# Optimization experiments

Measured on AMD Instinct MI355X. Metric: run time of the kernel, lower is better.

The kernel has to match this reference:

```python
import jax, jax.numpy as jnp
import numpy as np

DIM = 4096          # power of two -> no padding branch
LAYERS = 12         # log2(DIM)
BATCH = 8192


def setup_inputs() -> dict:
    key = jax.random.key(0)
    kx, ka = jax.random.split(key)
    x = jax.random.normal(kx, (BATCH, DIM), dtype=jnp.float32)
    # original init: uniform(-0.05, 0.05) per layer of DIM//2 angles
    angles = jax.random.uniform(ka, (LAYERS, DIM // 2), dtype=jnp.float32,
                                minval=-0.05, maxval=0.05)
    return {"x": x, "angles": angles}


def reference(x, angles):
    """Butterfly O(d log d) rotation. x:(B,d), angles:(L, d//2).

    Layer l pairs elements (j, j+stride), stride=2**l. The torch code's
    angle index for pair offset i in block starting at `start` is
    start//2 + i, which equals reshaping theta to (num_blocks, stride).
    """
    B, d = x.shape
    out = x
    for l in range(LAYERS):
        stride = 1 << l
        nb = d // (2 * stride)              # blocks per layer
        theta = angles[l].reshape(nb, stride)
        c = jnp.cos(theta)                  # (nb, stride)
        s = jnp.sin(theta)
        o = out.reshape(B, nb, 2, stride)
        xl = o[:, :, 0, :]                  # (B, nb, stride)
        xr = o[:, :, 1, :]
        new_l = c * xl + s * xr
        new_r = -s * xl + c * xr
        out = jnp.stack([new_l, new_r], axis=2).reshape(B, d)
    return out
```

## Files before the change

### kernel.cpp

```cpp
#include <hip/hip_runtime.h>
#include <hip/hip_fp16.h>


#define DIM    4096
#define LAYERS 12
#define BATCH  8192
#define NANG   2048
#define BLOCK  512

typedef unsigned int u32;
typedef float v2f __attribute__((ext_vector_type(2)));

#define BAR() do {                                             \
    asm volatile("s_waitcnt lgkmcnt(0)" ::: "memory");         \
    __builtin_amdgcn_sched_barrier(0);                         \
    __builtin_amdgcn_s_barrier();                              \
} while (0)

__device__ __forceinline__ int swzQ(int Q) {
    return Q ^ ((Q >> 3) & 7) ^ ((Q >> 6) & 7);
}
__device__ __forceinline__ int uslot(int e) {
    return 2 * swzQ(e >> 1) + (e & 1);
}
__device__ __forceinline__ constexpr int inner_idx(int m, int jj) {
    return ((m >> (jj + 1)) << jj) + (m & ((1 << jj) - 1));
}

__device__ __forceinline__ void rot2(v2f& xl, v2f& xr, float c, float s) {
    v2f nl = c * xl + s * xr;
    v2f nr = c * xr - s * xl;
    xl = nl; xr = nr;
}

__global__ void __launch_bounds__(256) cs_kernel(const float* __restrict__ angles,
                                                 u32* __restrict__ TH, int n) {
    int i = blockIdx.x * blockDim.x + threadIdx.x;
    if (i >= n) return;
    float a = angles[i];
    float c = cosf(a), s = sinf(a);
    int l = i >> 11, aa = i & 2047;
    int region, jj, t, ii;
    if (l < 3)      { region = 0; jj = l;     t = aa >> 2;  ii = aa & 3; }
    else if (l < 6) { region = 1; jj = l - 3; int B = aa >> 5, r = aa & 31;
                      ii = r >> 3; t = 8 * B + (r & 7); }
    else if (l < 9) { region = 2; jj = l - 6; int S = aa >> 8, r = aa & 255;
                      ii = r >> 6; t = 64 * S + (r & 63); }
    else            { region = 3; jj = l - 9; ii = aa >> 9; t = aa & 511; }
    int a_idx = jj * 4 + ii;
    int flat = ((region * 3 + (a_idx >> 2)) * 512 + t) * 4 + (a_idx & 3);
    u32 lo = (u32)__half_as_ushort(__float2half(1.0f - c));
    u32 hi = (u32)__half_as_ushort(__float2half(s));
    TH[flat] = lo | (hi << 16);
}

#define UNPACK_ANGLES(U0, U1, U2, ca, sa) do {                             \
    const u32 _u[12] = {U0.x, U0.y, U0.z, U0.w, U1.x, U1.y, U1.z, U1.w,    \
                        U2.x, U2.y, U2.z, U2.w};                           \
    _Pragma("unroll")                                                      \
    for (int a = 0; a < 12; ++a) {                                         \
        __half2 h2 = *reinterpret_cast<const __half2*>(&_u[a]);            \
        float2 f = __half22float2(h2);                                     \
        ca[a] = 1.0f - f.x;                                                \
        sa[a] = f.y;                                                       \
    }                                                                      \
} while (0)

#define PHASE_ROTS(ca, sa, w)                                              \
    _Pragma("unroll")                                                      \
    for (int jj = 0; jj < 3; ++jj) {                                       \
        const int st = 1 << jj;                                            \
        _Pragma("unroll")                                                  \
        for (int m = 0; m < 8; ++m) {                                      \
            if (!(m & st)) {                                               \
                const int a = jj * 4 + inner_idx(m, jj);                   \
                rot2(w[m], w[m + st], ca[a], sa[a]);                       \
            }                                                              \
        }                                                                  \
    }

__global__ void __launch_bounds__(BLOCK, 6)
butterfly_kernel(const float* __restrict__ x, const uint4* __restrict__ TH4,
                 float* __restrict__ out) {
    __shared__ v2f buf[DIM];
    const int t = threadIdx.x;
    const long row0 = (long)blockIdx.x * 2;

    v2f w[8];
    float ca[12], sa[12];

    {
        uint4 A0 = TH4[0 * 512 + t], A1 = TH4[1 * 512 + t], A2 = TH4[2 * 512 + t];
        const float* p0 = x + row0 * DIM + 8 * t;
        const float* p1 = p0 + DIM;
        float4 a = *(const float4*)(p0),     b = *(const float4*)(p0 + 4);
        float4 c = *(const float4*)(p1),     d = *(const float4*)(p1 + 4);
        uint4 B0 = TH4[3 * 512 + t], B1 = TH4[4 * 512 + t], B2 = TH4[5 * 512 + t];

        w[0] = v2f{a.x, c.x}; w[1] = v2f{a.y, c.y};
        w[2] = v2f{a.z, c.z}; w[3] = v2f{a.w, c.w};
        w[4] = v2f{b.x, d.x}; w[5] = v2f{b.y, d.y};
        w[6] = v2f{b.z, d.z}; w[7] = v2f{b.w, d.w};
        UNPACK_ANGLES(A0, A1, A2, ca, sa);
        PHASE_ROTS(ca, sa, w)
        #pragma unroll
        for (int q = 0; q < 4; ++q) {
            *(float4*)(&buf[2 * swzQ(4 * t + q)]) =
                make_float4(w[2*q].x, w[2*q].y, w[2*q+1].x, w[2*q+1].y);
        }
        BAR();

        uint4 C0 = TH4[6 * 512 + t], C1 = TH4[7 * 512 + t], C2 = TH4[8 * 512 + t];
        {
            const int eb = 64 * (t >> 3) + (t & 7);
            int ps[8];
            #pragma unroll
            for (int m = 0; m < 8; ++m) {
                ps[m] = uslot(eb + 8 * m);
                w[m] = buf[ps[m]];
            }
            UNPACK_ANGLES(B0, B1, B2, ca, sa);
            PHASE_ROTS(ca, sa, w)
            #pragma unroll
            for (int m = 0; m < 8; ++m) buf[ps[m]] = w[m];
        }
        BAR();

        uint4 D0 = TH4[9 * 512 + t], D1 = TH4[10 * 512 + t], D2 = TH4[11 * 512 + t];
        {
            const int eb = 512 * (t >> 6) + (t & 63);
            int ps[8];
            #pragma unroll
            for (int m = 0; m < 8; ++m) {
                ps[m] = uslot(eb + 64 * m);
                w[m] = buf[ps[m]];
            }
            UNPACK_ANGLES(C0, C1, C2, ca, sa);
            PHASE_ROTS(ca, sa, w)
            #pragma unroll
            for (int m = 0; m < 8; ++m) buf[ps[m]] = w[m];
        }
        BAR();

        {
            #pragma unroll
            for (int m = 0; m < 8; ++m) w[m] = buf[uslot(t + 512 * m)];
            UNPACK_ANGLES(D0, D1, D2, ca, sa);
            PHASE_ROTS(ca, sa, w)
            float* o0 = out + row0 * DIM + t;
            float* o1 = o0 + DIM;
            #pragma unroll
            for (int m = 0; m < 8; ++m) {
                o0[m << 9] = w[m].x;
                o1[m << 9] = w[m].y;
            }
        }
    }
}

extern "C" void kernel_launch(void* const* d_in, const int* in_sizes, int n_in,
                              void* d_out, int out_size, void* d_ws, size_t ws_size,
                              hipStream_t stream) {
    (void)in_sizes; (void)n_in; (void)out_size; (void)ws_size;
    const float* x      = (const float*)d_in[0];
    const float* angles = (const float*)d_in[1];
    float* out = (float*)d_out;

    const int n = LAYERS * NANG;
    cs_kernel<<<(n + 255) / 256, 256, 0, stream>>>(angles, (u32*)d_ws, n);
    butterfly_kernel<<<BATCH / 2, BLOCK, 0, stream>>>(x, (const uint4*)d_ws, out);
}
```

Baseline: 53.15 us.

## Use 16 elements per thread with 256-thread blocks and three LDS phases

Each thread now holds 16 two-row elements instead of 8, so each register phase covers four butterfly layers instead of three. The kernel needs three phases and two barriers instead of four phases and three, which cuts LDS round trips. Blocks shrink to 256 threads, and the angle table is re-laid out into 8 uint4 groups per phase. The rotation now uses the packed 1-cos value directly rather than rebuilding cos. More registers per thread lower the occupancy target from 6 to 4 blocks.

```diff
diff --git a/kernel.cpp b/kernel.cpp
--- a/kernel.cpp
+++ b/kernel.cpp
@@ -6,7 +6,7 @@
 #define LAYERS 12
 #define BATCH  8192
 #define NANG   2048
-#define BLOCK  512
+#define BLOCK  256
 
 typedef unsigned int u32;
 typedef float v2f __attribute__((ext_vector_type(2)));
@@ -27,9 +27,11 @@
     return ((m >> (jj + 1)) << jj) + (m & ((1 << jj) - 1));
 }
 
-__device__ __forceinline__ void rot2(v2f& xl, v2f& xr, float c, float s) {
-    v2f nl = c * xl + s * xr;
-    v2f nr = c * xr - s * xl;
+__device__ __forceinline__ void rot2d(v2f& xl, v2f& xr, float d, float s) {
+    v2f cl = xl - d * xl;
+    v2f cr = xr - d * xr;
+    v2f nl = cl + s * xr;
+    v2f nr = cr - s * xl;
     xl = nl; xr = nr;
 }
 
@@ -41,119 +43,107 @@
     float c = cosf(a), s = sinf(a);
     int l = i >> 11, aa = i & 2047;
     int region, jj, t, ii;
-    if (l < 3)      { region = 0; jj = l;     t = aa >> 2;  ii = aa & 3; }
-    else if (l < 6) { region = 1; jj = l - 3; int B = aa >> 5, r = aa & 31;
-                      ii = r >> 3; t = 8 * B + (r & 7); }
-    else if (l < 9) { region = 2; jj = l - 6; int S = aa >> 8, r = aa & 255;
-                      ii = r >> 6; t = 64 * S + (r & 63); }
-    else            { region = 3; jj = l - 9; ii = aa >> 9; t = aa & 511; }
-    int a_idx = jj * 4 + ii;
-    int flat = ((region * 3 + (a_idx >> 2)) * 512 + t) * 4 + (a_idx & 3);
+    if (l < 4)      { region = 0; jj = l;     t = aa >> 3; ii = aa & 7; }
+    else if (l < 8) { region = 1; jj = l - 4; int hi = aa >> 7, r = aa & 127;
+                      ii = r >> 4; t = hi + 16 * (r & 15); }
+    else            { region = 2; jj = l - 8; ii = aa >> 8; t = aa & 255; }
+    int group = region * 8 + jj * 2 + (ii >> 2);
+    int flat = (group * 256 + t) * 4 + (ii & 3);
     u32 lo = (u32)__half_as_ushort(__float2half(1.0f - c));
     u32 hi = (u32)__half_as_ushort(__float2half(s));
     TH[flat] = lo | (hi << 16);
 }
 
-#define UNPACK_ANGLES(U0, U1, U2, ca, sa) do {                             \
-    const u32 _u[12] = {U0.x, U0.y, U0.z, U0.w, U1.x, U1.y, U1.z, U1.w,    \
-                        U2.x, U2.y, U2.z, U2.w};                           \
+#define UNPACK8(Ua, Ub, dd, ss) do {                                       \
+    const u32 _u[8] = {Ua.x, Ua.y, Ua.z, Ua.w, Ub.x, Ub.y, Ub.z, Ub.w};    \
     _Pragma("unroll")                                                      \
-    for (int a = 0; a < 12; ++a) {                                         \
+    for (int a = 0; a < 8; ++a) {                                          \
         __half2 h2 = *reinterpret_cast<const __half2*>(&_u[a]);            \
         float2 f = __half22float2(h2);                                     \
-        ca[a] = 1.0f - f.x;                                                \
-        sa[a] = f.y;                                                       \
+        dd[a] = f.x; ss[a] = f.y;                                          \
     }                                                                      \
 } while (0)
 
-#define PHASE_ROTS(ca, sa, w)                                              \
+#define PHASE_ROTS(U, w)                                                   \
     _Pragma("unroll")                                                      \
-    for (int jj = 0; jj < 3; ++jj) {                                       \
+    for (int jj = 0; jj < 4; ++jj) {                                       \
+        float dd[8], ss[8];                                                \
+        UNPACK8(U[2*jj], U[2*jj+1], dd, ss);                               \
         const int st = 1 << jj;                                            \
         _Pragma("unroll")                                                  \
-        for (int m = 0; m < 8; ++m) {                                      \
+        for (int m = 0; m < 16; ++m) {                                     \
             if (!(m & st)) {                                               \
-                const int a = jj * 4 + inner_idx(m, jj);                   \
-                rot2(w[m], w[m + st], ca[a], sa[a]);                       \
+                rot2d(w[m], w[m + st], dd[inner_idx(m, jj)],               \
+                      ss[inner_idx(m, jj)]);                               \
             }                                                              \
         }                                                                  \
     }
 
-__global__ void __launch_bounds__(BLOCK, 6)
+__global__ void __launch_bounds__(BLOCK, 4)
 butterfly_kernel(const float* __restrict__ x, const uint4* __restrict__ TH4,
                  float* __restrict__ out) {
     __shared__ v2f buf[DIM];
     const int t = threadIdx.x;
     const long row0 = (long)blockIdx.x * 2;
 
-    v2f w[8];
-    float ca[12], sa[12];
+    v2f w[16];
+    uint4 U[8];
 
     {
-        uint4 A0 = TH4[0 * 512 + t], A1 = TH4[1 * 512 + t], A2 = TH4[2 * 512 + t];
-        const float* p0 = x + row0 * DIM + 8 * t;
+        const float* p0 = x + row0 * DIM + 16 * t;
         const float* p1 = p0 + DIM;
-        float4 a = *(const float4*)(p0),     b = *(const float4*)(p0 + 4);
-        float4 c = *(const float4*)(p1),     d = *(const float4*)(p1 + 4);
-        uint4 B0 = TH4[3 * 512 + t], B1 = TH4[4 * 512 + t], B2 = TH4[5 * 512 + t];
-
-        w[0] = v2f{a.x, c.x}; w[1] = v2f{a.y, c.y};
-        w[2] = v2f{a.z, c.z}; w[3] = v2f{a.w, c.w};
-        w[4] = v2f{b.x, d.x}; w[5] = v2f{b.y, d.y};
-        w[6] = v2f{b.z, d.z}; w[7] = v2f{b.w, d.w};
-        UNPACK_ANGLES(A0, A1, A2, ca, sa);
-        PHASE_ROTS(ca, sa, w)
+        float4 r0q[4], r1q[4];
         #pragma unroll
         for (int q = 0; q < 4; ++q) {
-            *(float4*)(&buf[2 * swzQ(4 * t + q)]) =
-                make_float4(w[2*q].x, w[2*q].y, w[2*q+1].x, w[2*q+1].y);
+            r0q[q] = *(const float4*)(p0 + 4 * q);
+            r1q[q] = *(const float4*)(p1 + 4 * q);
         }
-        BAR();
+        #pragma unroll
+        for (int q = 0; q < 8; ++q) U[q] = TH4[q * 256 + t];
+        #pragma unroll
+        for (int q = 0; q < 4; ++q) {
+            w[4*q+0] = v2f{r0q[q].x, r1q[q].x};
+            w[4*q+1] = v2f{r0q[q].y, r1q[q].y};
+            w[4*q+2] = v2f{r0q[q].z, r1q[q].z};
+            w[4*q+3] = v2f{r0q[q].w, r1q[q].w};
+        }
+        PHASE_ROTS(U, w)
+        #pragma unroll
+        for (int q = 0; q < 8; ++q) U[q] = TH4[(8 + q) * 256 + t];
+        #pragma unroll
+        for (int wq = 0; wq < 8; ++wq) {
+            *(float4*)(&buf[2 * swzQ(8 * t + wq)]) =
+                make_float4(w[2*wq].x, w[2*wq].y, w[2*wq+1].x, w[2*wq+1].y);
+        }
+    }
+    BAR();
 
-        uint4 C0 = TH4[6 * 512 + t], C1 = TH4[7 * 512 + t], C2 = TH4[8 * 512 + t];
-        {
-            const int eb = 64 * (t >> 3) + (t & 7);
-            int ps[8];
-            #pragma unroll
-            for (int m = 0; m < 8; ++m) {
-                ps[m] = uslot(eb + 8 * m);
-                w[m] = buf[ps[m]];
-            }
-            UNPACK_ANGLES(B0, B1, B2, ca, sa);
-            PHASE_ROTS(ca, sa, w)
-            #pragma unroll
-            for (int m = 0; m < 8; ++m) buf[ps[m]] = w[m];
+    {
+        const int hi = t & 15, lo = t >> 4;
+        int ps[16];
+        #pragma unroll
+        for (int m = 0; m < 16; ++m) {
+            ps[m] = uslot((hi << 8) + (m << 4) + lo);
+            w[m] = buf[ps[m]];
         }
-        BAR();
+        PHASE_ROTS(U, w)
+        #pragma unroll
+        for (int q = 0; q < 8; ++q) U[q] = TH4[(16 + q) * 256 + t];
+        #pragma unroll
+        for (int m = 0; m < 16; ++m) buf[ps[m]] = w[m];
+    }
+    BAR();
 
-        uint4 D0 = TH4[9 * 512 + t], D1 = TH4[10 * 512 + t], D2 = TH4[11 * 512 + t];
-        {
-            const int eb = 512 * (t >> 6) + (t & 63);
-            int ps[8];
-            #pragma unroll
-            for (int m = 0; m < 8; ++m) {
-                ps[m] = uslot(eb + 64 * m);
-                w[m] = buf[ps[m]];
-            }
-            UNPACK_ANGLES(C0, C1, C2, ca, sa);
-            PHASE_ROTS(ca, sa, w)
-            #pragma unroll
-            for (int m = 0; m < 8; ++m) buf[ps[m]] = w[m];
-        }
-        BAR();
-
-        {
-            #pragma unroll
-            for (int m = 0; m < 8; ++m) w[m] = buf[uslot(t + 512 * m)];
-            UNPACK_ANGLES(D0, D1, D2, ca, sa);
-            PHASE_ROTS(ca, sa, w)
-            float* o0 = out + row0 * DIM + t;
-            float* o1 = o0 + DIM;
-            #pragma unroll
-            for (int m = 0; m < 8; ++m) {
-                o0[m << 9] = w[m].x;
-                o1[m << 9] = w[m].y;
-            }
+    {
+        #pragma unroll
+        for (int m = 0; m < 16; ++m) w[m] = buf[uslot(t + (m << 8))];
+        PHASE_ROTS(U, w)
+        float* o0 = out + row0 * DIM + t;
+        float* o1 = o0 + DIM;
+        #pragma unroll
+        for (int m = 0; m < 16; ++m) {
+            o0[m << 8] = w[m].x;
+            o1[m << 8] = w[m].y;
         }
     }
 }
```

Result: slower. 91.63 us (+72.4%).

## Process two row pairs per block and prefetch next pair's inputs during rotations

Applied to the files above, without the earlier changes.

Each block now handles four rows as two sequential row-pair iterations, halving the grid. The next pair's x data is loaded during the third phase of the first pair, overlapping global loads with LDS butterfly work. The angle tables are reloaded for the second pass. The rotation is reformulated to use the stored (1-c) value directly as x - d*x + s*y, avoiding the 1-f subtraction. A trailing barrier is added, and the halved grid reduces block-level parallelism and raises register pressure.

```diff
diff --git a/kernel.cpp b/kernel.cpp
--- a/kernel.cpp
+++ b/kernel.cpp
@@ -7,6 +7,7 @@
 #define BATCH  8192
 #define NANG   2048
 #define BLOCK  512
+#define GRID   (BATCH / 4)
 
 typedef unsigned int u32;
 typedef float v2f __attribute__((ext_vector_type(2)));
@@ -27,9 +28,11 @@
     return ((m >> (jj + 1)) << jj) + (m & ((1 << jj) - 1));
 }
 
-__device__ __forceinline__ void rot2(v2f& xl, v2f& xr, float c, float s) {
-    v2f nl = c * xl + s * xr;
-    v2f nr = c * xr - s * xl;
+__device__ __forceinline__ void rot2d(v2f& xl, v2f& xr, float d, float s) {
+    v2f cl = xl - d * xl;
+    v2f cr = xr - d * xr;
+    v2f nl = cl + s * xr;
+    v2f nr = cr - s * xl;
     xl = nl; xr = nr;
 }
 
@@ -54,19 +57,18 @@
     TH[flat] = lo | (hi << 16);
 }
 
-#define UNPACK_ANGLES(U0, U1, U2, ca, sa) do {                             \
-    const u32 _u[12] = {U0.x, U0.y, U0.z, U0.w, U1.x, U1.y, U1.z, U1.w,    \
-                        U2.x, U2.y, U2.z, U2.w};                           \
+#define UNPACK12(Ua, Ub, Uc, dd, ss) do {                                  \
+    const u32 _u[12] = {Ua.x, Ua.y, Ua.z, Ua.w, Ub.x, Ub.y, Ub.z, Ub.w,    \
+                        Uc.x, Uc.y, Uc.z, Uc.w};                           \
     _Pragma("unroll")                                                      \
     for (int a = 0; a < 12; ++a) {                                         \
         __half2 h2 = *reinterpret_cast<const __half2*>(&_u[a]);            \
         float2 f = __half22float2(h2);                                     \
-        ca[a] = 1.0f - f.x;                                                \
-        sa[a] = f.y;                                                       \
+        dd[a] = f.x; ss[a] = f.y;                                          \
     }                                                                      \
 } while (0)
 
-#define PHASE_ROTS(ca, sa, w)                                              \
+#define PHASE_ROTS(dd, ss, w)                                              \
     _Pragma("unroll")                                                      \
     for (int jj = 0; jj < 3; ++jj) {                                       \
         const int st = 1 << jj;                                            \
@@ -74,7 +76,7 @@
         for (int m = 0; m < 8; ++m) {                                      \
             if (!(m & st)) {                                               \
                 const int a = jj * 4 + inner_idx(m, jj);                   \
-                rot2(w[m], w[m + st], ca[a], sa[a]);                       \
+                rot2d(w[m], w[m + st], dd[a], ss[a]);                      \
             }                                                              \
         }                                                                  \
     }
@@ -84,34 +86,48 @@
                  float* __restrict__ out) {
     __shared__ v2f buf[DIM];
     const int t = threadIdx.x;
-    const long row0 = (long)blockIdx.x * 2;
+    const long base = (long)blockIdx.x * 4;
 
     v2f w[8];
-    float ca[12], sa[12];
+    float dd[12], ss[12];
+    float4 xa0, xa1, xa2, xa3;
+    float4 xb0, xb1, xb2, xb3;
+    uint4 U0, U1, U2;
 
     {
-        uint4 A0 = TH4[0 * 512 + t], A1 = TH4[1 * 512 + t], A2 = TH4[2 * 512 + t];
-        const float* p0 = x + row0 * DIM + 8 * t;
-        const float* p1 = p0 + DIM;
-        float4 a = *(const float4*)(p0),     b = *(const float4*)(p0 + 4);
-        float4 c = *(const float4*)(p1),     d = *(const float4*)(p1 + 4);
-        uint4 B0 = TH4[3 * 512 + t], B1 = TH4[4 * 512 + t], B2 = TH4[5 * 512 + t];
-
-        w[0] = v2f{a.x, c.x}; w[1] = v2f{a.y, c.y};
-        w[2] = v2f{a.z, c.z}; w[3] = v2f{a.w, c.w};
-        w[4] = v2f{b.x, d.x}; w[5] = v2f{b.y, d.y};
-        w[6] = v2f{b.z, d.z}; w[7] = v2f{b.w, d.w};
-        UNPACK_ANGLES(A0, A1, A2, ca, sa);
-        PHASE_ROTS(ca, sa, w)
-        #pragma unroll
-        for (int q = 0; q < 4; ++q) {
-            *(float4*)(&buf[2 * swzQ(4 * t + q)]) =
-                make_float4(w[2*q].x, w[2*q].y, w[2*q+1].x, w[2*q+1].y);
-        }
-        BAR();
-
-        uint4 C0 = TH4[6 * 512 + t], C1 = TH4[7 * 512 + t], C2 = TH4[8 * 512 + t];
-        {
+        const float* p0 = x + base * DIM + 8 * t;
+        xa0 = *(const float4*)(p0);
+        xa1 = *(const float4*)(p0 + 4);
+        xa2 = *(const float4*)(p0 + DIM);
+        xa3 = *(const float4*)(p0 + DIM + 4);
+        U0 = TH4[0 * 512 + t]; U1 = TH4[1 * 512 + t]; U2 = TH4[2 * 512 + t];
+    }
+
+    #pragma unroll
+    for (int q = 0; q < 2; ++q) {
+        {
+            float4 a = (q == 0) ? xa0 : xb0;
+            float4 b = (q == 0) ? xa1 : xb1;
+            float4 c = (q == 0) ? xa2 : xb2;
+            float4 d = (q == 0) ? xa3 : xb3;
+            uint4 V0 = TH4[3 * 512 + t], V1 = TH4[4 * 512 + t], V2 = TH4[5 * 512 + t];
+            w[0] = v2f{a.x, c.x}; w[1] = v2f{a.y, c.y};
+            w[2] = v2f{a.z, c.z}; w[3] = v2f{a.w, c.w};
+            w[4] = v2f{b.x, d.x}; w[5] = v2f{b.y, d.y};
+            w[6] = v2f{b.z, d.z}; w[7] = v2f{b.w, d.w};
+            UNPACK12(U0, U1, U2, dd, ss);
+            PHASE_ROTS(dd, ss, w)
+            #pragma unroll
+            for (int wq = 0; wq < 4; ++wq) {
+                *(float4*)(&buf[2 * swzQ(4 * t + wq)]) =
+                    make_float4(w[2*wq].x, w[2*wq].y, w[2*wq+1].x, w[2*wq+1].y);
+            }
+            U0 = V0; U1 = V1; U2 = V2;
+        }
+        BAR();
+
+        {
+            uint4 V0 = TH4[6 * 512 + t], V1 = TH4[7 * 512 + t], V2 = TH4[8 * 512 + t];
             const int eb = 64 * (t >> 3) + (t & 7);
             int ps[8];
             #pragma unroll
@@ -119,15 +135,23 @@
                 ps[m] = uslot(eb + 8 * m);
                 w[m] = buf[ps[m]];
             }
-            UNPACK_ANGLES(B0, B1, B2, ca, sa);
-            PHASE_ROTS(ca, sa, w)
+            UNPACK12(U0, U1, U2, dd, ss);
+            PHASE_ROTS(dd, ss, w)
             #pragma unroll
             for (int m = 0; m < 8; ++m) buf[ps[m]] = w[m];
-        }
-        BAR();
-
-        uint4 D0 = TH4[9 * 512 + t], D1 = TH4[10 * 512 + t], D2 = TH4[11 * 512 + t];
-        {
+            U0 = V0; U1 = V1; U2 = V2;
+        }
+        BAR();
+
+        {
+            uint4 V0 = TH4[9 * 512 + t], V1 = TH4[10 * 512 + t], V2 = TH4[11 * 512 + t];
+            if (q == 0) {
+                const float* p1 = x + (base + 2) * DIM + 8 * t;
+                xb0 = *(const float4*)(p1);
+                xb1 = *(const float4*)(p1 + 4);
+                xb2 = *(const float4*)(p1 + DIM);
+                xb3 = *(const float4*)(p1 + DIM + 4);
+            }
             const int eb = 512 * (t >> 6) + (t & 63);
             int ps[8];
             #pragma unroll
@@ -135,26 +159,33 @@
                 ps[m] = uslot(eb + 64 * m);
                 w[m] = buf[ps[m]];
             }
-            UNPACK_ANGLES(C0, C1, C2, ca, sa);
-            PHASE_ROTS(ca, sa, w)
+            UNPACK12(U0, U1, U2, dd, ss);
+            PHASE_ROTS(dd, ss, w)
             #pragma unroll
             for (int m = 0; m < 8; ++m) buf[ps[m]] = w[m];
-        }
-        BAR();
-
-        {
+            U0 = V0; U1 = V1; U2 = V2;
+        }
+        BAR();
+
+        {
+            uint4 V0, V1, V2;
+            if (q == 0) {
+                V0 = TH4[0 * 512 + t]; V1 = TH4[1 * 512 + t]; V2 = TH4[2 * 512 + t];
+            }
             #pragma unroll
             for (int m = 0; m < 8; ++m) w[m] = buf[uslot(t + 512 * m)];
-            UNPACK_ANGLES(D0, D1, D2, ca, sa);
-            PHASE_ROTS(ca, sa, w)
-            float* o0 = out + row0 * DIM + t;
+            UNPACK12(U0, U1, U2, dd, ss);
+            PHASE_ROTS(dd, ss, w)
+            float* o0 = out + (base + 2 * q) * DIM + t;
             float* o1 = o0 + DIM;
             #pragma unroll
             for (int m = 0; m < 8; ++m) {
                 o0[m << 9] = w[m].x;
                 o1[m << 9] = w[m].y;
             }
-        }
+            if (q == 0) { U0 = V0; U1 = V1; U2 = V2; }
+        }
+        BAR();
     }
 }
 
@@ -168,5 +199,5 @@
 
     const int n = LAYERS * NANG;
     cs_kernel<<<(n + 255) / 256, 256, 0, stream>>>(angles, (u32*)d_ws, n);
-    butterfly_kernel<<<BATCH / 2, BLOCK, 0, stream>>>(x, (const uint4*)d_ws, out);
-}
+    butterfly_kernel<<<GRID, BLOCK, 0, stream>>>(x, (const uint4*)d_ws, out);
+}
```

After: 179.7 us. +238.0%, slower.
